# Kernel tuning notes

Hardware: AMD Instinct MI355X
Metric: run time of the kernel (lower is better)

## Reference

```python
import jax, jax.numpy as jnp
import numpy as np

INPUT, HIDDEN = 15, 20

def setup_inputs() -> dict:
    key = jax.random.key(0)
    k1, k2, k3, k4, k5 = jax.random.split(key, 5)
    B, T = 4096, 512
    s = 1.0 / np.sqrt(HIDDEN)  # torch default uniform init bound
    feature = jax.random.normal(k1, (B, T, INPUT), dtype=jnp.float32)
    W_ih = jax.random.uniform(k2, (HIDDEN, INPUT), jnp.float32, -s, s)
    W_hh = jax.random.uniform(k3, (HIDDEN, HIDDEN), jnp.float32, -s, s)
    b_ih = jax.random.uniform(k4, (HIDDEN,), jnp.float32, -s, s)
    b_hh = jax.random.uniform(k5, (HIDDEN,), jnp.float32, -s, s)
    return {"feature": feature, "W_ih": W_ih, "W_hh": W_hh, "b_ih": b_ih, "b_hh": b_hh}

def reference(feature, W_ih, W_hh, b_ih, b_hh):
    # h_t = tanh(x_t @ W_ih^T + b_ih + h_{t-1} @ W_hh^T + b_hh)
    B, T, _ = feature.shape
    # precompute input projections for all timesteps: [T, B, H]
    xp = jnp.einsum('bti,hi->tbh', feature, W_ih) + (b_ih + b_hh)
    h0 = jnp.zeros((B, HIDDEN), dtype=feature.dtype)
    def step(h, x_t):
        h_new = jnp.tanh(x_t + h @ W_hh.T)
        return h_new, None
    hn, _ = jax.lax.scan(step, h0, xp)
    return hn  # [B, H] == hn.squeeze() for num_layers=1
```

## Files before the change

### kernel.cpp

```cpp
#include <hip/hip_runtime.h>
#include <cstddef>


typedef float g4 __attribute__((ext_vector_type(4), aligned(4)));
typedef float g2 __attribute__((ext_vector_type(2), aligned(4)));
typedef float v4 __attribute__((ext_vector_type(4)));
typedef float f2 __attribute__((ext_vector_type(2)));

#define TT 512
#define IN 15
#define HD 20
#define CH 32
#define NCH (TT / CH)

__device__ __forceinline__ f2 lo2(v4 v) { return (f2){v.x, v.y}; }
__device__ __forceinline__ f2 hi2(v4 v) { return (f2){v.z, v.w}; }

__global__ __launch_bounds__(64) void rnn_fused(
    const float* __restrict__ feature, const float* __restrict__ W_ih,
    const float* __restrict__ W_hh, const float* __restrict__ b_ih,
    const float* __restrict__ b_hh, float* __restrict__ out, int B) {
  __shared__ float xb[2][3][CH][16];
  __shared__ float hl[4][HD];

  const int lane = threadIdx.x;
  const int g = lane / HD;
  const int j = lane - g * HD;
  const int gx = (g < 3) ? g : 2;
  const int bid = blockIdx.x;
  const int b = bid * 3 + g;

  for (int i = lane; i < 4 * HD; i += 64) ((float*)hl)[i] = 0.f;
  for (int i = lane; i < 2 * 3 * CH; i += 64) ((float*)xb)[i * 16 + 15] = 0.f;

  f2 wih[8];
  {
    const float* wr = W_ih + j * IN;
#pragma unroll
    for (int i = 0; i < 7; ++i) wih[i] = (f2){wr[2 * i], wr[2 * i + 1]};
    wih[7] = (f2){wr[14], 0.f};
  }
  f2 whh[10];
  {
    const float* wr = W_hh + j * HD;
#pragma unroll
    for (int i = 0; i < 10; ++i) whh[i] = (f2){wr[2 * i], wr[2 * i + 1]};
  }
  const float bias = b_ih[j] + b_hh[j];

  const int grA = lane >> 5;
  const int tcA = lane & 31;
  const int bc = B - 1;
  const int bA = min(bid * 3 + grA, bc);
  const int bB = min(bid * 3 + 2, bc);
  const float* baseA = feature + ((size_t)bA * TT + tcA) * IN;
  const float* baseB = feature + ((size_t)bB * TT + tcA) * IN;

  g4 rA0, rA1, rA2; g2 rA3; float rA4;
  g4 rB0, rB1, rB2; g2 rB3; float rB4;

  auto issue = [&](int t0) {
    const float* s = baseA + (size_t)t0 * IN;
    rA0 = *(const g4*)(s);      rA1 = *(const g4*)(s + 4);
    rA2 = *(const g4*)(s + 8);  rA3 = *(const g2*)(s + 12);
    rA4 = s[14];
    if (lane < 32) {
      const float* s2 = baseB + (size_t)t0 * IN;
      rB0 = *(const g4*)(s2);     rB1 = *(const g4*)(s2 + 4);
      rB2 = *(const g4*)(s2 + 8); rB3 = *(const g2*)(s2 + 12);
      rB4 = s2[14];
    }
  };
  auto commit = [&](int bsel) {
    float* d = &xb[bsel][grA][tcA][0];
    *(v4*)d = (v4)rA0; *(v4*)(d + 4) = (v4)rA1; *(v4*)(d + 8) = (v4)rA2;
    *(f2*)(d + 12) = (f2)rA3; d[14] = rA4;
    if (lane < 32) {
      float* d2 = &xb[bsel][2][tcA][0];
      *(v4*)d2 = (v4)rB0; *(v4*)(d2 + 4) = (v4)rB1; *(v4*)(d2 + 8) = (v4)rB2;
      *(f2*)(d2 + 12) = (f2)rB3; d2[14] = rB4;
    }
  };

  issue(0);
  commit(0);

  float hn = 0.f;
  const float* hrow = &hl[g][0];
  float* hwr = &hl[g][j];
  for (int c = 0; c < NCH; ++c) {
    if (c + 1 < NCH) issue((c + 1) * CH);
    const float* xrow = &xb[c & 1][gx][0][0];
#pragma unroll 4
    for (int tc = 0; tc < CH; ++tc) {
      const v4* xp = (const v4*)(xrow + tc * 16);
      v4 x0 = xp[0], x1 = xp[1], x2 = xp[2], x3 = xp[3];
      const v4* hp = (const v4*)hrow;
      v4 h0 = hp[0], h1 = hp[1], h2 = hp[2], h3 = hp[3], h4 = hp[4];
      f2 a0 = (f2){bias, 0.f}, a1 = (f2){0.f, 0.f};
      f2 a2 = (f2){0.f, 0.f},  a3 = (f2){0.f, 0.f};
      a0 += lo2(x0) * wih[0]; a1 += hi2(x0) * wih[1];
      a2 += lo2(x1) * wih[2]; a3 += hi2(x1) * wih[3];
      a0 += lo2(x2) * wih[4]; a1 += hi2(x2) * wih[5];
      a2 += lo2(x3) * wih[6]; a3 += hi2(x3) * wih[7];
      a0 += lo2(h0) * whh[0]; a1 += hi2(h0) * whh[1];
      a2 += lo2(h1) * whh[2]; a3 += hi2(h1) * whh[3];
      a0 += lo2(h2) * whh[4]; a1 += hi2(h2) * whh[5];
      a2 += lo2(h3) * whh[6]; a3 += hi2(h3) * whh[7];
      a0 += lo2(h4) * whh[8]; a1 += hi2(h4) * whh[9];
      f2 sv = (a0 + a1) + (a2 + a3);
      float s = sv.x + sv.y;
      float e = exp2f(s * 2.8853900817779268f);
      hn = 1.f - 2.f * __builtin_amdgcn_rcpf(1.f + e);
      *hwr = hn;
    }
    if (c + 1 < NCH) commit((c + 1) & 1);
  }
  if (g < 3 && b < B) out[(size_t)b * HD + j] = hn;
}

extern "C" void kernel_launch(void* const* d_in, const int* in_sizes, int n_in,
                              void* d_out, int out_size, void* d_ws, size_t ws_size,
                              hipStream_t stream) {
  const float* feature = (const float*)d_in[0];
  const float* W_ih    = (const float*)d_in[1];
  const float* W_hh    = (const float*)d_in[2];
  const float* b_ih    = (const float*)d_in[3];
  const float* b_hh    = (const float*)d_in[4];
  float* out = (float*)d_out;
  const int B = in_sizes[0] / (TT * IN);
  const int grid = (B + 2) / 3;
  rnn_fused<<<grid, 64, 0, stream>>>(feature, W_ih, W_hh, b_ih, b_hh, out, B);
}
```

Baseline: 241.7 us.

## Rewrite RNN kernel with DPP row-rotate recurrence and fp16 dot2 input projection

```diff
diff --git a/kernel.cpp b/kernel.cpp
--- a/kernel.cpp
+++ b/kernel.cpp
@@ -4,119 +4,159 @@
 
 typedef float g4 __attribute__((ext_vector_type(4), aligned(4)));
 typedef float g2 __attribute__((ext_vector_type(2), aligned(4)));
-typedef float v4 __attribute__((ext_vector_type(4)));
-typedef float f2 __attribute__((ext_vector_type(2)));
+typedef float v4f __attribute__((ext_vector_type(4)));
+typedef __fp16 h2t __attribute__((ext_vector_type(2)));
+typedef __fp16 v16h __attribute__((ext_vector_type(16)));
 
 #define TT 512
 #define IN 15
 #define HD 20
 #define CH 32
 #define NCH (TT / CH)
+#define XPS 25
+#define GS (32 * XPS + 8)
 
-__device__ __forceinline__ f2 lo2(v4 v) { return (f2){v.x, v.y}; }
-__device__ __forceinline__ f2 hi2(v4 v) { return (f2){v.z, v.w}; }
+#define HH(acc, h, w, R)                                                     \
+  asm("v_fmac_f32 %0, %1, %2 row_ror:" #R " row_mask:0xf bank_mask:0xf"      \
+      : "+v"(acc) : "v"(h), "v"(w))
 
-__global__ __launch_bounds__(64) void rnn_fused(
+#define FDI(i)                                                               \
+  {                                                                          \
+    h2t wp = __builtin_shufflevector(wv, wv, 2 * (i), 2 * (i) + 1);          \
+    a = __builtin_amdgcn_fdot2(xa[i], wp, a, false);                         \
+    c = __builtin_amdgcn_fdot2(xb[i], wp, c, false);                         \
+  }
+
+__global__ __launch_bounds__(64, 1) void rnn_dpp(
     const float* __restrict__ feature, const float* __restrict__ W_ih,
     const float* __restrict__ W_hh, const float* __restrict__ b_ih,
-    const float* __restrict__ b_hh, float* __restrict__ out, int B) {
-  __shared__ float xb[2][3][CH][16];
-  __shared__ float hl[4][HD];
+    const float* __restrict__ b_hh, float* __restrict__ out) {
+  __shared__ float xpL[4 * GS + 40];
+  __shared__ __fp16 wihL[HD][16];
 
   const int lane = threadIdx.x;
-  const int g = lane / HD;
-  const int j = lane - g * HD;
-  const int gx = (g < 3) ? g : 2;
-  const int bid = blockIdx.x;
-  const int b = bid * 3 + g;
+  const int g = lane >> 4;
+  const int k = lane & 15;
+  const int b = blockIdx.x * 4 + g;
 
-  for (int i = lane; i < 4 * HD; i += 64) ((float*)hl)[i] = 0.f;
-  for (int i = lane; i < 2 * 3 * CH; i += 64) ((float*)xb)[i * 16 + 15] = 0.f;
+  if (lane < HD) {
+    const float* wr = W_ih + lane * IN;
+#pragma unroll
+    for (int i = 0; i < IN; ++i) wihL[lane][i] = (__fp16)wr[i];
+    wihL[lane][15] = (__fp16)(b_ih[lane] + b_hh[lane]);
+  }
 
-  f2 wih[8];
-  {
-    const float* wr = W_ih + j * IN;
+  const int probe = __builtin_amdgcn_update_dpp(0, k, 0x121, 0xf, 0xf, true);
+  const bool plus = (probe == ((k + 1) & 15));
+
+  const int j2 = 16 + (k & 3);
+  float wA1[16], wB1[16], wA2[4], wB2[4];
 #pragma unroll
-    for (int i = 0; i < 7; ++i) wih[i] = (f2){wr[2 * i], wr[2 * i + 1]};
-    wih[7] = (f2){wr[14], 0.f};
+  for (int r = 0; r < 16; ++r) {
+    const int s = (plus ? (k + r) : (k - r)) & 15;
+    wA1[r] = W_hh[k * HD + s];
+    wB1[r] = W_hh[j2 * HD + s];
   }
-  f2 whh[10];
-  {
-    const float* wr = W_hh + j * HD;
 #pragma unroll
-    for (int i = 0; i < 10; ++i) whh[i] = (f2){wr[2 * i], wr[2 * i + 1]};
+  for (int r = 0; r < 4; ++r) {
+    const int s = 16 + ((plus ? (k + r) : (k - r)) & 3);
+    wA2[r] = W_hh[k * HD + s];
+    wB2[r] = W_hh[j2 * HD + s];
   }
-  const float bias = b_ih[j] + b_hh[j];
 
-  const int grA = lane >> 5;
-  const int tcA = lane & 31;
-  const int bc = B - 1;
-  const int bA = min(bid * 3 + grA, bc);
-  const int bB = min(bid * 3 + 2, bc);
-  const float* baseA = feature + ((size_t)bA * TT + tcA) * IN;
-  const float* baseB = feature + ((size_t)bB * TT + tcA) * IN;
-
+  const float* rb = feature + ((size_t)b * TT) * IN;
   g4 rA0, rA1, rA2; g2 rA3; float rA4;
   g4 rB0, rB1, rB2; g2 rB3; float rB4;
+  auto issue = [&](int t0) {
+    const float* s = rb + (size_t)(t0 + k) * IN;
+    rA0 = *(const g4*)(s);      rA1 = *(const g4*)(s + 4);
+    rA2 = *(const g4*)(s + 8);  rA3 = *(const g2*)(s + 12);  rA4 = s[14];
+    const float* s2 = rb + (size_t)(t0 + 16 + k) * IN;
+    rB0 = *(const g4*)(s2);     rB1 = *(const g4*)(s2 + 4);
+    rB2 = *(const g4*)(s2 + 8); rB3 = *(const g2*)(s2 + 12); rB4 = s2[14];
+  };
 
-  auto issue = [&](int t0) {
-    const float* s = baseA + (size_t)t0 * IN;
-    rA0 = *(const g4*)(s);      rA1 = *(const g4*)(s + 4);
-    rA2 = *(const g4*)(s + 8);  rA3 = *(const g2*)(s + 12);
-    rA4 = s[14];
-    if (lane < 32) {
-      const float* s2 = baseB + (size_t)t0 * IN;
-      rB0 = *(const g4*)(s2);     rB1 = *(const g4*)(s2 + 4);
-      rB2 = *(const g4*)(s2 + 8); rB3 = *(const g2*)(s2 + 12);
-      rB4 = s2[14];
-    }
-  };
-  auto commit = [&](int bsel) {
-    float* d = &xb[bsel][grA][tcA][0];
-    *(v4*)d = (v4)rA0; *(v4*)(d + 4) = (v4)rA1; *(v4*)(d + 8) = (v4)rA2;
-    *(f2*)(d + 12) = (f2)rA3; d[14] = rA4;
-    if (lane < 32) {
-      float* d2 = &xb[bsel][2][tcA][0];
-      *(v4*)d2 = (v4)rB0; *(v4*)(d2 + 4) = (v4)rB1; *(v4*)(d2 + 8) = (v4)rB2;
-      *(f2*)(d2 + 12) = (f2)rB3; d2[14] = rB4;
+  auto do_xp = [&]() {
+    h2t xa[8], xb[8];
+    xa[0] = __builtin_amdgcn_cvt_pkrtz(rA0.x, rA0.y);
+    xa[1] = __builtin_amdgcn_cvt_pkrtz(rA0.z, rA0.w);
+    xa[2] = __builtin_amdgcn_cvt_pkrtz(rA1.x, rA1.y);
+    xa[3] = __builtin_amdgcn_cvt_pkrtz(rA1.z, rA1.w);
+    xa[4] = __builtin_amdgcn_cvt_pkrtz(rA2.x, rA2.y);
+    xa[5] = __builtin_amdgcn_cvt_pkrtz(rA2.z, rA2.w);
+    xa[6] = __builtin_amdgcn_cvt_pkrtz(rA3.x, rA3.y);
+    xa[7] = __builtin_amdgcn_cvt_pkrtz(rA4, 1.0f);
+    xb[0] = __builtin_amdgcn_cvt_pkrtz(rB0.x, rB0.y);
+    xb[1] = __builtin_amdgcn_cvt_pkrtz(rB0.z, rB0.w);
+    xb[2] = __builtin_amdgcn_cvt_pkrtz(rB1.x, rB1.y);
+    xb[3] = __builtin_amdgcn_cvt_pkrtz(rB1.z, rB1.w);
+    xb[4] = __builtin_amdgcn_cvt_pkrtz(rB2.x, rB2.y);
+    xb[5] = __builtin_amdgcn_cvt_pkrtz(rB2.z, rB2.w);
+    xb[6] = __builtin_amdgcn_cvt_pkrtz(rB3.x, rB3.y);
+    xb[7] = __builtin_amdgcn_cvt_pkrtz(rB4, 1.0f);
+    float* d1 = xpL + g * GS + k * XPS;
+    float* d2 = xpL + g * GS + (16 + k) * XPS;
+#pragma unroll
+    for (int j0 = 0; j0 < HD; j0 += 4) {
+      v4f bufA, bufB;
+#pragma unroll
+      for (int jj = 0; jj < 4; ++jj) {
+        v16h wv = *(const v16h*)&wihL[j0 + jj][0];
+        float a = 0.f, c = 0.f;
+        FDI(0) FDI(1) FDI(2) FDI(3) FDI(4) FDI(5) FDI(6) FDI(7)
+        bufA[jj] = a; bufB[jj] = c;
+      }
+      *(v4f*)(d1 + j0) = bufA;
+      *(v4f*)(d2 + j0) = bufB;
     }
   };
 
   issue(0);
-  commit(0);
+  do_xp();
 
-  float hn = 0.f;
-  const float* hrow = &hl[g][0];
-  float* hwr = &hl[g][j];
+  float h1 = 0.f, h2v = 0.f;
+  const float* xr1 = xpL + g * GS + k;
+  const float* xr2 = xpL + g * GS + 16 + (k & 3);
+
   for (int c = 0; c < NCH; ++c) {
     if (c + 1 < NCH) issue((c + 1) * CH);
-    const float* xrow = &xb[c & 1][gx][0][0];
+    float p1 = xr1[0], p2 = xr2[0];
 #pragma unroll 4
-    for (int tc = 0; tc < CH; ++tc) {
-      const v4* xp = (const v4*)(xrow + tc * 16);
-      v4 x0 = xp[0], x1 = xp[1], x2 = xp[2], x3 = xp[3];
-      const v4* hp = (const v4*)hrow;
-      v4 h0 = hp[0], h1 = hp[1], h2 = hp[2], h3 = hp[3], h4 = hp[4];
-      f2 a0 = (f2){bias, 0.f}, a1 = (f2){0.f, 0.f};
-      f2 a2 = (f2){0.f, 0.f},  a3 = (f2){0.f, 0.f};
-      a0 += lo2(x0) * wih[0]; a1 += hi2(x0) * wih[1];
-      a2 += lo2(x1) * wih[2]; a3 += hi2(x1) * wih[3];
-      a0 += lo2(x2) * wih[4]; a1 += hi2(x2) * wih[5];
-      a2 += lo2(x3) * wih[6]; a3 += hi2(x3) * wih[7];
-      a0 += lo2(h0) * whh[0]; a1 += hi2(h0) * whh[1];
-      a2 += lo2(h1) * whh[2]; a3 += hi2(h1) * whh[3];
-      a0 += lo2(h2) * whh[4]; a1 += hi2(h2) * whh[5];
-      a2 += lo2(h3) * whh[6]; a3 += hi2(h3) * whh[7];
-      a0 += lo2(h4) * whh[8]; a1 += hi2(h4) * whh[9];
-      f2 sv = (a0 + a1) + (a2 + a3);
-      float s = sv.x + sv.y;
-      float e = exp2f(s * 2.8853900817779268f);
-      hn = 1.f - 2.f * __builtin_amdgcn_rcpf(1.f + e);
-      *hwr = hn;
+    for (int t = 0; t < CH; ++t) {
+      float a0 = p1, a1 = 0.f, b0 = p2, b1 = 0.f;
+      p1 = xr1[(t + 1) * XPS];
+      p2 = xr2[(t + 1) * XPS];
+      a0 = fmaf(h1, wA1[0], a0);  b0 = fmaf(h1, wB1[0], b0);
+      HH(a1, h1, wA1[1], 1);   HH(b1, h1, wB1[1], 1);
+      HH(a0, h1, wA1[2], 2);   HH(b0, h1, wB1[2], 2);
+      HH(a1, h1, wA1[3], 3);   HH(b1, h1, wB1[3], 3);
+      HH(a0, h1, wA1[4], 4);   HH(b0, h1, wB1[4], 4);
+      HH(a1, h1, wA1[5], 5);   HH(b1, h1, wB1[5], 5);
+      HH(a0, h1, wA1[6], 6);   HH(b0, h1, wB1[6], 6);
+      HH(a1, h1, wA1[7], 7);   HH(b1, h1, wB1[7], 7);
+      HH(a0, h1, wA1[8], 8);   HH(b0, h1, wB1[8], 8);
+      HH(a1, h1, wA1[9], 9);   HH(b1, h1, wB1[9], 9);
+      HH(a0, h1, wA1[10], 10); HH(b0, h1, wB1[10], 10);
+      HH(a1, h1, wA1[11], 11); HH(b1, h1, wB1[11], 11);
+      HH(a0, h1, wA1[12], 12); HH(b0, h1, wB1[12], 12);
+      HH(a1, h1, wA1[13], 13); HH(b1, h1, wB1[13], 13);
+      HH(a0, h1, wA1[14], 14); HH(b0, h1, wB1[14], 14);
+      HH(a1, h1, wA1[15], 15); HH(b1, h1, wB1[15], 15);
+      a0 = fmaf(h2v, wA2[0], a0); b0 = fmaf(h2v, wB2[0], b0);
+      HH(a1, h2v, wA2[1], 1); HH(b1, h2v, wB2[1], 1);
+      HH(a0, h2v, wA2[2], 2); HH(b0, h2v, wB2[2], 2);
+      HH(a1, h2v, wA2[3], 3); HH(b1, h2v, wB2[3], 3);
+      const float s1 = a0 + a1, s2 = b0 + b1;
+      const float e1 = exp2f(s1 * 2.8853900817779268f);
+      const float e2 = exp2f(s2 * 2.8853900817779268f);
+      h1  = 1.f - 2.f * __builtin_amdgcn_rcpf(1.f + e1);
+      h2v = 1.f - 2.f * __builtin_amdgcn_rcpf(1.f + e2);
     }
-    if (c + 1 < NCH) commit((c + 1) & 1);
+    if (c + 1 < NCH) do_xp();
   }
-  if (g < 3 && b < B) out[(size_t)b * HD + j] = hn;
+
+  out[(size_t)b * HD + k] = h1;
+  if (k < 4) out[(size_t)b * HD + 16 + k] = h2v;
 }
 
 extern "C" void kernel_launch(void* const* d_in, const int* in_sizes, int n_in,
@@ -129,6 +169,5 @@
   const float* b_hh    = (const float*)d_in[4];
   float* out = (float*)d_out;
   const int B = in_sizes[0] / (TT * IN);
-  const int grid = (B + 2) / 3;
-  rnn_fused<<<grid, 64, 0, stream>>>(feature, W_ih, W_hh, b_ih, b_hh, out, B);
+  rnn_dpp<<<B / 4, 64, 0, stream>>>(feature, W_ih, W_hh, b_ih, b_hh, out);
 }
```

Result: slower. 252.6 us (+4.5%).

## Rewrite RNN recurrence with fp16 MFMA over 16 sequences per wavefront

Applied to the files above, without the earlier changes.

```diff
diff --git a/kernel.cpp b/kernel.cpp
--- a/kernel.cpp
+++ b/kernel.cpp
@@ -3,120 +3,137 @@
 
 
 typedef float g4 __attribute__((ext_vector_type(4), aligned(4)));
-typedef float g2 __attribute__((ext_vector_type(2), aligned(4)));
-typedef float v4 __attribute__((ext_vector_type(4)));
-typedef float f2 __attribute__((ext_vector_type(2)));
+typedef float v4f __attribute__((ext_vector_type(4)));
+typedef _Float16 v8h __attribute__((ext_vector_type(8)));
+typedef int vi4 __attribute__((ext_vector_type(4)));
 
 #define TT 512
 #define IN 15
 #define HD 20
-#define CH 32
+#define CH 8
 #define NCH (TT / CH)
 
-__device__ __forceinline__ f2 lo2(v4 v) { return (f2){v.x, v.y}; }
-__device__ __forceinline__ f2 hi2(v4 v) { return (f2){v.z, v.w}; }
+#define MFMA16(a, b, c) __builtin_amdgcn_mfma_f32_16x16x32_f16(a, b, c, 0, 0, 0)
 
-__global__ __launch_bounds__(64) void rnn_fused(
+__device__ __forceinline__ int pk(float lo, float hi) {
+  return __builtin_bit_cast(int, __builtin_amdgcn_cvt_pkrtz(lo, hi));
+}
+__device__ __forceinline__ float tanh_fast(float s) {
+  float e = exp2f(s * 2.8853900817779268f);
+  return __builtin_fmaf(__builtin_amdgcn_rcpf(1.f + e), -2.f, 1.f);
+}
+
+__global__ __launch_bounds__(64, 1) void rnn_mfma(
     const float* __restrict__ feature, const float* __restrict__ W_ih,
     const float* __restrict__ W_hh, const float* __restrict__ b_ih,
-    const float* __restrict__ b_hh, float* __restrict__ out, int B) {
-  __shared__ float xb[2][3][CH][16];
-  __shared__ float hl[4][HD];
+    const float* __restrict__ b_hh, float* __restrict__ out) {
+  const int lane = threadIdx.x;
+  const int n = lane & 15;
+  const int q = lane >> 4;
+  const bool qodd = (q & 1) != 0;
+  const bool isQ2 = (q == 2);
+  const int b = blockIdx.x * 16 + n;
 
-  const int lane = threadIdx.x;
-  const int g = lane / HD;
-  const int j = lane - g * HD;
-  const int gx = (g < 3) ? g : 2;
-  const int bid = blockIdx.x;
-  const int b = bid * 3 + g;
+  vi4 A1i, A2i, Xai, Xbi;
+  {
+    const int k0 = q * 8;
+#pragma unroll
+    for (int d = 0; d < 4; ++d) {
+      const int k = k0 + 2 * d;
+      const float w0 = (k < HD) ? W_hh[n * HD + k] : 0.f;
+      const float w1 = (k + 1 < HD) ? W_hh[n * HD + k + 1] : 0.f;
+      A1i[d] = pk(w0, w1);
+      const float v0 = (n < 4 && k < HD) ? W_hh[(16 + n) * HD + k] : 0.f;
+      const float v1 = (n < 4 && k + 1 < HD) ? W_hh[(16 + n) * HD + k + 1] : 0.f;
+      A2i[d] = pk(v0, v1);
+      const float x0 = (k < IN) ? W_ih[n * IN + k] : 0.f;
+      const float x1 = (k + 1 < IN) ? W_ih[n * IN + k + 1] : 0.f;
+      Xai[d] = pk(x0, x1);
+      const float y0 = (n < 4 && k < IN) ? W_ih[(16 + n) * IN + k] : 0.f;
+      const float y1 = (n < 4 && k + 1 < IN) ? W_ih[(16 + n) * IN + k + 1] : 0.f;
+      Xbi[d] = pk(y0, y1);
+    }
+  }
+  const v8h A1 = __builtin_bit_cast(v8h, A1i);
+  const v8h A2 = __builtin_bit_cast(v8h, A2i);
+  const v8h Xa = __builtin_bit_cast(v8h, Xai);
+  const v8h Xb = __builtin_bit_cast(v8h, Xbi);
 
-  for (int i = lane; i < 4 * HD; i += 64) ((float*)hl)[i] = 0.f;
-  for (int i = lane; i < 2 * 3 * CH; i += 64) ((float*)xb)[i * 16 + 15] = 0.f;
+  v4f Cba, Cbb;
+#pragma unroll
+  for (int r = 0; r < 4; ++r) {
+    const int j = 4 * q + r;
+    Cba[r] = b_ih[j] + b_hh[j];
+    Cbb[r] = (q == 0) ? (b_ih[16 + r] + b_hh[16 + r]) : 0.f;
+  }
 
-  f2 wih[8];
-  {
-    const float* wr = W_ih + j * IN;
+  const int a0 = 4 * (n + ((q == 1) ? 32 : 0));
+  const int a2 = 4 * (n + 16 + ((q == 1) ? 32 : 0));
+  const int aE = 4 * n;
+
+  const float* fbase = feature + ((size_t)b * TT) * IN + (qodd ? 7 : 0);
+  g4 flo[CH], fhi[CH];
+  auto issueF = [&](int t0) {
 #pragma unroll
-    for (int i = 0; i < 7; ++i) wih[i] = (f2){wr[2 * i], wr[2 * i + 1]};
-    wih[7] = (f2){wr[14], 0.f};
-  }
-  f2 whh[10];
-  {
-    const float* wr = W_hh + j * HD;
-#pragma unroll
-    for (int i = 0; i < 10; ++i) whh[i] = (f2){wr[2 * i], wr[2 * i + 1]};
-  }
-  const float bias = b_ih[j] + b_hh[j];
-
-  const int grA = lane >> 5;
-  const int tcA = lane & 31;
-  const int bc = B - 1;
-  const int bA = min(bid * 3 + grA, bc);
-  const int bB = min(bid * 3 + 2, bc);
-  const float* baseA = feature + ((size_t)bA * TT + tcA) * IN;
-  const float* baseB = feature + ((size_t)bB * TT + tcA) * IN;
-
-  g4 rA0, rA1, rA2; g2 rA3; float rA4;
-  g4 rB0, rB1, rB2; g2 rB3; float rB4;
-
-  auto issue = [&](int t0) {
-    const float* s = baseA + (size_t)t0 * IN;
-    rA0 = *(const g4*)(s);      rA1 = *(const g4*)(s + 4);
-    rA2 = *(const g4*)(s + 8);  rA3 = *(const g2*)(s + 12);
-    rA4 = s[14];
-    if (lane < 32) {
-      const float* s2 = baseB + (size_t)t0 * IN;
-      rB0 = *(const g4*)(s2);     rB1 = *(const g4*)(s2 + 4);
-      rB2 = *(const g4*)(s2 + 8); rB3 = *(const g2*)(s2 + 12);
-      rB4 = s2[14];
-    }
-  };
-  auto commit = [&](int bsel) {
-    float* d = &xb[bsel][grA][tcA][0];
-    *(v4*)d = (v4)rA0; *(v4*)(d + 4) = (v4)rA1; *(v4*)(d + 8) = (v4)rA2;
-    *(f2*)(d + 12) = (f2)rA3; d[14] = rA4;
-    if (lane < 32) {
-      float* d2 = &xb[bsel][2][tcA][0];
-      *(v4*)d2 = (v4)rB0; *(v4*)(d2 + 4) = (v4)rB1; *(v4*)(d2 + 8) = (v4)rB2;
-      *(f2*)(d2 + 12) = (f2)rB3; d2[14] = rB4;
+    for (int tt = 0; tt < CH; ++tt) {
+      const float* s = fbase + (size_t)(t0 + tt) * IN;
+      flo[tt] = *(const g4*)s;
+      fhi[tt] = *(const g4*)(s + 4);
     }
   };
 
-  issue(0);
-  commit(0);
+  v4f xpa[CH], xpb[CH];
+  auto doXP = [&]() {
+#pragma unroll
+    for (int tt = 0; tt < CH; ++tt) {
+      const g4 lo = flo[tt], hi = fhi[tt];
+      const int d0 = qodd ? pk(lo.y, lo.z) : pk(lo.x, lo.y);
+      const int d1 = qodd ? pk(lo.w, hi.x) : pk(lo.z, lo.w);
+      const int d2 = qodd ? pk(hi.y, hi.z) : pk(hi.x, hi.y);
+      const int d3 = qodd ? pk(hi.w, 0.f) : pk(hi.z, hi.w);
+      const v8h Bx = __builtin_bit_cast(v8h, (vi4){d0, d1, d2, d3});
+      xpa[tt] = MFMA16(Xa, Bx, Cba);
+      xpb[tt] = MFMA16(Xb, Bx, Cbb);
+    }
+  };
 
-  float hn = 0.f;
-  const float* hrow = &hl[g][0];
-  float* hwr = &hl[g][j];
+  issueF(0);
+  doXP();
+
+  vi4 Bi = {0, 0, 0, 0};
+  float T0 = 0.f, T1 = 0.f, T2 = 0.f, T3 = 0.f;
+  float U0 = 0.f, U1 = 0.f, U2 = 0.f, U3 = 0.f;
+
   for (int c = 0; c < NCH; ++c) {
-    if (c + 1 < NCH) issue((c + 1) * CH);
-    const float* xrow = &xb[c & 1][gx][0][0];
-#pragma unroll 4
-    for (int tc = 0; tc < CH; ++tc) {
-      const v4* xp = (const v4*)(xrow + tc * 16);
-      v4 x0 = xp[0], x1 = xp[1], x2 = xp[2], x3 = xp[3];
-      const v4* hp = (const v4*)hrow;
-      v4 h0 = hp[0], h1 = hp[1], h2 = hp[2], h3 = hp[3], h4 = hp[4];
-      f2 a0 = (f2){bias, 0.f}, a1 = (f2){0.f, 0.f};
-      f2 a2 = (f2){0.f, 0.f},  a3 = (f2){0.f, 0.f};
-      a0 += lo2(x0) * wih[0]; a1 += hi2(x0) * wih[1];
-      a2 += lo2(x1) * wih[2]; a3 += hi2(x1) * wih[3];
-      a0 += lo2(x2) * wih[4]; a1 += hi2(x2) * wih[5];
-      a2 += lo2(x3) * wih[6]; a3 += hi2(x3) * wih[7];
-      a0 += lo2(h0) * whh[0]; a1 += hi2(h0) * whh[1];
-      a2 += lo2(h1) * whh[2]; a3 += hi2(h1) * whh[3];
-      a0 += lo2(h2) * whh[4]; a1 += hi2(h2) * whh[5];
-      a2 += lo2(h3) * whh[6]; a3 += hi2(h3) * whh[7];
-      a0 += lo2(h4) * whh[8]; a1 += hi2(h4) * whh[9];
-      f2 sv = (a0 + a1) + (a2 + a3);
-      float s = sv.x + sv.y;
-      float e = exp2f(s * 2.8853900817779268f);
-      hn = 1.f - 2.f * __builtin_amdgcn_rcpf(1.f + e);
-      *hwr = hn;
+    if (c + 1 < NCH) issueF((c + 1) * CH);
+#pragma unroll
+    for (int tt = 0; tt < CH; ++tt) {
+      const v8h B = __builtin_bit_cast(v8h, Bi);
+      const v4f Da = MFMA16(A1, B, xpa[tt]);
+      const v4f Db = MFMA16(A2, B, xpb[tt]);
+      T0 = tanh_fast(Da.x); T1 = tanh_fast(Da.y);
+      T2 = tanh_fast(Da.z); T3 = tanh_fast(Da.w);
+      U0 = tanh_fast(Db.x); U1 = tanh_fast(Db.y);
+      U2 = tanh_fast(Db.z); U3 = tanh_fast(Db.w);
+      const int P0 = pk(T0, T1), P1 = pk(T2, T3);
+      const int E0 = pk(U0, U1), E1 = pk(U2, U3);
+      const int g0 = __builtin_amdgcn_ds_bpermute(a0, P0);
+      const int g0e = __builtin_amdgcn_ds_bpermute(aE, E0);
+      const int g1 = __builtin_amdgcn_ds_bpermute(a0, P1);
+      const int g1e = __builtin_amdgcn_ds_bpermute(aE, E1);
+      const int d2 = __builtin_amdgcn_ds_bpermute(a2, P0);
+      const int d3 = __builtin_amdgcn_ds_bpermute(a2, P1);
+      Bi = (vi4){isQ2 ? g0e : g0, isQ2 ? g1e : g1, d2, d3};
     }
-    if (c + 1 < NCH) commit((c + 1) & 1);
+    if (c + 1 < NCH) doXP();
   }
-  if (g < 3 && b < B) out[(size_t)b * HD + j] = hn;
+
+  float* ob = out + (size_t)b * HD + 4 * q;
+  ob[0] = T0; ob[1] = T1; ob[2] = T2; ob[3] = T3;
+  if (q == 0) {
+    float* o2 = out + (size_t)b * HD + 16;
+    o2[0] = U0; o2[1] = U1; o2[2] = U2; o2[3] = U3;
+  }
 }
 
 extern "C" void kernel_launch(void* const* d_in, const int* in_sizes, int n_in,
@@ -129,6 +146,5 @@
   const float* b_hh    = (const float*)d_in[4];
   float* out = (float*)d_out;
   const int B = in_sizes[0] / (TT * IN);
-  const int grid = (B + 2) / 3;
-  rnn_fused<<<grid, 64, 0, stream>>>(feature, W_ih, W_hh, b_ih, b_hh, out, B);
+  rnn_mfma<<<B / 16, 64, 0, stream>>>(feature, W_ih, W_hh, b_ih, b_hh, out);
 }
```

New measurement: 298.6 us. +23.6%, slower.

## Use fp16 dot2 for RNN step and prefetch inputs directly into registers

Applied to the files above, without the earlier changes.

```diff
diff --git a/kernel.cpp b/kernel.cpp
--- a/kernel.cpp
+++ b/kernel.cpp
@@ -3,118 +3,100 @@
 
 
 typedef float g4 __attribute__((ext_vector_type(4), aligned(4)));
-typedef float g2 __attribute__((ext_vector_type(2), aligned(4)));
-typedef float v4 __attribute__((ext_vector_type(4)));
-typedef float f2 __attribute__((ext_vector_type(2)));
+typedef __fp16 h2t __attribute__((ext_vector_type(2)));
+typedef __fp16 v8h __attribute__((ext_vector_type(8)));
+typedef __fp16 v4h __attribute__((ext_vector_type(4)));
 
 #define TT 512
 #define IN 15
 #define HD 20
-#define CH 32
-#define NCH (TT / CH)
+#define PF 4
 
-__device__ __forceinline__ f2 lo2(v4 v) { return (f2){v.x, v.y}; }
-__device__ __forceinline__ f2 hi2(v4 v) { return (f2){v.z, v.w}; }
+#define PK(a, b) __builtin_amdgcn_cvt_pkrtz((a), (b))
+#define FD(acc, p, w) acc = __builtin_amdgcn_fdot2((p), (w), (acc), false)
+#define SH(v, i) __builtin_shufflevector((v), (v), 2 * (i), 2 * (i) + 1)
 
-__global__ __launch_bounds__(64) void rnn_fused(
+__device__ __forceinline__ float tanh_fast(float s) {
+  const float e = exp2f(s * 2.8853900817779268f);
+  return __builtin_fmaf(__builtin_amdgcn_rcpf(1.f + e), -2.f, 1.f);
+}
+
+__global__ __launch_bounds__(64, 1) void rnn_v5(
     const float* __restrict__ feature, const float* __restrict__ W_ih,
     const float* __restrict__ W_hh, const float* __restrict__ b_ih,
     const float* __restrict__ b_hh, float* __restrict__ out, int B) {
-  __shared__ float xb[2][3][CH][16];
-  __shared__ float hl[4][HD];
+  __shared__ __fp16 hl[4 * 24];
 
   const int lane = threadIdx.x;
   const int g = lane / HD;
   const int j = lane - g * HD;
-  const int gx = (g < 3) ? g : 2;
-  const int bid = blockIdx.x;
-  const int b = bid * 3 + g;
+  const int b = blockIdx.x * 3 + g;
+  const int bck = min(b, B - 1);
 
-  for (int i = lane; i < 4 * HD; i += 64) ((float*)hl)[i] = 0.f;
-  for (int i = lane; i < 2 * 3 * CH; i += 64) ((float*)xb)[i * 16 + 15] = 0.f;
+  if (lane < 48) ((float*)hl)[lane] = 0.f;
 
-  f2 wih[8];
+  h2t wih[8];
   {
     const float* wr = W_ih + j * IN;
 #pragma unroll
-    for (int i = 0; i < 7; ++i) wih[i] = (f2){wr[2 * i], wr[2 * i + 1]};
-    wih[7] = (f2){wr[14], 0.f};
+    for (int i = 0; i < 7; ++i) wih[i] = PK(wr[2 * i], wr[2 * i + 1]);
+    wih[7] = PK(wr[14], 0.f);
   }
-  f2 whh[10];
+  h2t whh[10];
   {
-    const float* wr = W_hh + j * HD;
+    const float* wq = W_hh + j * HD;
 #pragma unroll
-    for (int i = 0; i < 10; ++i) whh[i] = (f2){wr[2 * i], wr[2 * i + 1]};
+    for (int i = 0; i < 10; ++i) whh[i] = PK(wq[2 * i], wq[2 * i + 1]);
   }
   const float bias = b_ih[j] + b_hh[j];
 
-  const int grA = lane >> 5;
-  const int tcA = lane & 31;
-  const int bc = B - 1;
-  const int bA = min(bid * 3 + grA, bc);
-  const int bB = min(bid * 3 + 2, bc);
-  const float* baseA = feature + ((size_t)bA * TT + tcA) * IN;
-  const float* baseB = feature + ((size_t)bB * TT + tcA) * IN;
+  const float* rb = feature + (size_t)bck * TT * IN;
 
-  g4 rA0, rA1, rA2; g2 rA3; float rA4;
-  g4 rB0, rB1, rB2; g2 rB3; float rB4;
+  g4 xs[PF][4];
+#pragma unroll
+  for (int p = 0; p < PF; ++p) {
+    const float* s = rb + (size_t)p * IN;
+    xs[p][0] = *(const g4*)s;       xs[p][1] = *(const g4*)(s + 4);
+    xs[p][2] = *(const g4*)(s + 8); xs[p][3] = *(const g4*)(s + 11);
+  }
 
-  auto issue = [&](int t0) {
-    const float* s = baseA + (size_t)t0 * IN;
-    rA0 = *(const g4*)(s);      rA1 = *(const g4*)(s + 4);
-    rA2 = *(const g4*)(s + 8);  rA3 = *(const g2*)(s + 12);
-    rA4 = s[14];
-    if (lane < 32) {
-      const float* s2 = baseB + (size_t)t0 * IN;
-      rB0 = *(const g4*)(s2);     rB1 = *(const g4*)(s2 + 4);
-      rB2 = *(const g4*)(s2 + 8); rB3 = *(const g2*)(s2 + 12);
-      rB4 = s2[14];
+  const __fp16* hr = hl + g * 24;
+  __fp16* hw = hl + g * 24 + j;
+  float hn = 0.f;
+
+#pragma unroll 1
+  for (int it = 0; it < TT / PF; ++it) {
+#pragma unroll
+    for (int p = 0; p < PF; ++p) {
+      const int t = it * PF + p;
+      const v8h hA = *(const v8h*)hr;
+      const v8h hB = *(const v8h*)(hr + 8);
+      const v4h hC = *(const v4h*)(hr + 16);
+      const g4 x0 = xs[p][0], x1 = xs[p][1], x2 = xs[p][2], x3 = xs[p][3];
+      {
+        int tn = t + PF; tn = (tn < TT) ? tn : (TT - 1);
+        const float* s = rb + (size_t)tn * IN;
+        xs[p][0] = *(const g4*)s;       xs[p][1] = *(const g4*)(s + 4);
+        xs[p][2] = *(const g4*)(s + 8); xs[p][3] = *(const g4*)(s + 11);
+      }
+      const h2t p0 = PK(x0.x, x0.y), p1 = PK(x0.z, x0.w);
+      const h2t p2 = PK(x1.x, x1.y), p3 = PK(x1.z, x1.w);
+      const h2t p4 = PK(x2.x, x2.y), p5 = PK(x2.z, x2.w);
+      const h2t p6 = PK(x3.y, x3.z), p7 = PK(x3.w, 0.f);
+      float a0 = bias, a1 = 0.f;
+      FD(a0, p0, wih[0]); FD(a1, p1, wih[1]);
+      FD(a0, p2, wih[2]); FD(a1, p3, wih[3]);
+      FD(a0, p4, wih[4]); FD(a1, p5, wih[5]);
+      FD(a0, p6, wih[6]); FD(a1, p7, wih[7]);
+      float b0 = 0.f, b1 = 0.f;
+      FD(b0, SH(hA, 0), whh[0]); FD(b1, SH(hA, 1), whh[1]);
+      FD(b0, SH(hA, 2), whh[2]); FD(b1, SH(hA, 3), whh[3]);
+      FD(b0, SH(hB, 0), whh[4]); FD(b1, SH(hB, 1), whh[5]);
+      FD(b0, SH(hB, 2), whh[6]); FD(b1, SH(hB, 3), whh[7]);
+      FD(b0, SH(hC, 0), whh[8]); FD(b1, SH(hC, 1), whh[9]);
+      hn = tanh_fast((a0 + a1) + (b0 + b1));
+      *hw = (__fp16)hn;
     }
-  };
-  auto commit = [&](int bsel) {
-    float* d = &xb[bsel][grA][tcA][0];
-    *(v4*)d = (v4)rA0; *(v4*)(d + 4) = (v4)rA1; *(v4*)(d + 8) = (v4)rA2;
-    *(f2*)(d + 12) = (f2)rA3; d[14] = rA4;
-    if (lane < 32) {
-      float* d2 = &xb[bsel][2][tcA][0];
-      *(v4*)d2 = (v4)rB0; *(v4*)(d2 + 4) = (v4)rB1; *(v4*)(d2 + 8) = (v4)rB2;
-      *(f2*)(d2 + 12) = (f2)rB3; d2[14] = rB4;
-    }
-  };
-
-  issue(0);
-  commit(0);
-
-  float hn = 0.f;
-  const float* hrow = &hl[g][0];
-  float* hwr = &hl[g][j];
-  for (int c = 0; c < NCH; ++c) {
-    if (c + 1 < NCH) issue((c + 1) * CH);
-    const float* xrow = &xb[c & 1][gx][0][0];
-#pragma unroll 4
-    for (int tc = 0; tc < CH; ++tc) {
-      const v4* xp = (const v4*)(xrow + tc * 16);
-      v4 x0 = xp[0], x1 = xp[1], x2 = xp[2], x3 = xp[3];
-      const v4* hp = (const v4*)hrow;
-      v4 h0 = hp[0], h1 = hp[1], h2 = hp[2], h3 = hp[3], h4 = hp[4];
-      f2 a0 = (f2){bias, 0.f}, a1 = (f2){0.f, 0.f};
-      f2 a2 = (f2){0.f, 0.f},  a3 = (f2){0.f, 0.f};
-      a0 += lo2(x0) * wih[0]; a1 += hi2(x0) * wih[1];
-      a2 += lo2(x1) * wih[2]; a3 += hi2(x1) * wih[3];
-      a0 += lo2(x2) * wih[4]; a1 += hi2(x2) * wih[5];
-      a2 += lo2(x3) * wih[6]; a3 += hi2(x3) * wih[7];
-      a0 += lo2(h0) * whh[0]; a1 += hi2(h0) * whh[1];
-      a2 += lo2(h1) * whh[2]; a3 += hi2(h1) * whh[3];
-      a0 += lo2(h2) * whh[4]; a1 += hi2(h2) * whh[5];
-      a2 += lo2(h3) * whh[6]; a3 += hi2(h3) * whh[7];
-      a0 += lo2(h4) * whh[8]; a1 += hi2(h4) * whh[9];
-      f2 sv = (a0 + a1) + (a2 + a3);
-      float s = sv.x + sv.y;
-      float e = exp2f(s * 2.8853900817779268f);
-      hn = 1.f - 2.f * __builtin_amdgcn_rcpf(1.f + e);
-      *hwr = hn;
-    }
-    if (c + 1 < NCH) commit((c + 1) & 1);
   }
   if (g < 3 && b < B) out[(size_t)b * HD + j] = hn;
 }
@@ -130,5 +112,5 @@
   float* out = (float*)d_out;
   const int B = in_sizes[0] / (TT * IN);
   const int grid = (B + 2) / 3;
-  rnn_fused<<<grid, 64, 0, stream>>>(feature, W_ih, W_hh, b_ih, b_hh, out, B);
+  rnn_v5<<<grid, 64, 0, stream>>>(feature, W_ih, W_hh, b_ih, b_hh, out, B);
 }
```

New measurement: 286.3 us. +18.5%, slower.
